# Kernel optimization log

Hardware: AMD Instinct MI355X
Metric: run time of the kernel (lower is better)

## Reference

```python
import jax, jax.numpy as jnp
import numpy as np

# dims
B_, L_, D_ = 2, 4096, 1024
E_ = 2
DIN = E_ * D_          # 2048 inner channels
P_ = 64                # d_head
H_ = DIN // P_         # 32 heads
N_ = 16                # d_state
K_ = 4                 # d_conv
DPROJ = 2 * DIN + 2 * N_ + H_   # z, u, B, C, dt
CONVD = DIN + 2 * N_            # conv over (u, B, C)


def rms(x, w, eps=1e-6):
    return x * jax.lax.rsqrt(jnp.mean(x * x, -1, keepdims=True) + eps) * w


def mixer(x, in_proj_w, conv_w, conv_b, A_param, dt_bias, D_skip, out_proj_w, out_proj_b):
    b, l, _ = x.shape
    proj = x @ in_proj_w.T                                   # (b,l,DPROJ)
    zgate, u, Bc, Cc, dt = jnp.split(proj, [DIN, 2 * DIN, 2 * DIN + N_, 2 * DIN + 2 * N_], axis=-1)
    # causal depthwise conv over (u,B,C), then SiLU
    xBC = jnp.concatenate([u, Bc, Cc], -1)                   # (b,l,CONVD)
    xt = jnp.pad(xBC.transpose(0, 2, 1), ((0, 0), (0, 0), (K_ - 1, 0)))
    conv = jax.lax.conv_general_dilated(xt, conv_w, (1,), 'VALID',
                                        feature_group_count=CONVD,
                                        dimension_numbers=('NCH', 'OIH', 'NCH'))
    xBC = jax.nn.silu(conv.transpose(0, 2, 1) + conv_b)
    u, Bc, Cc = jnp.split(xBC, [DIN, DIN + N_], axis=-1)
    # normalize_bc=True: L2-normalize B and C over the state dim
    Bc = Bc * jax.lax.rsqrt(jnp.sum(Bc * Bc, -1, keepdims=True) + 1e-6)
    Cc = Cc * jax.lax.rsqrt(jnp.sum(Cc * Cc, -1, keepdims=True) + 1e-6)
    dt = jax.nn.softplus(dt + dt_bias)                       # (b,l,H) selective step size
    A = jax.nn.relu(A_param)[None, :, None, :]               # (1,H,1,N) oscillator stiffness >= 0
    uh = u.reshape(b, l, H_, P_)

    def step(carry, inp):
        z, y = carry                                         # (b,H,P,N) each
        dt_t, B_t, C_t, u_t = inp
        d = dt_t[:, :, None, None]                           # (b,H,1,1)
        Bu = u_t[..., None] * B_t[:, None, None, :]          # (b,H,P,N)
        # LinOSS-IM implicit update (unconditionally stable)
        z = (z + d * (Bu - A * y)) / (1.0 + d * d * A)
        y = y + d * z
        out = jnp.einsum('bhpn,bn->bhp', y, C_t)
        return (z, y), out

    z0 = jnp.zeros((b, H_, P_, N_), x.dtype)
    seq = (dt.transpose(1, 0, 2), Bc.transpose(1, 0, 2), Cc.transpose(1, 0, 2), uh.transpose(1, 0, 2, 3))
    _, ys = jax.lax.scan(step, (z0, jnp.zeros_like(z0)), seq)  # (l,b,H,P)
    yout = ys.transpose(1, 0, 2, 3) + D_skip[None, None, :, None] * uh
    yout = yout.reshape(b, l, DIN) * jax.nn.silu(zgate)
    return yout @ out_proj_w.T + out_proj_b


def block_forward(x, norm1_w, in_proj_w, conv_w, conv_b, A_param, dt_bias, D_skip,
                  out_proj_w, out_proj_b, norm2_w, fc1_w, fc1_b, fc2_w, fc2_b):
    x = x + mixer(rms(x, norm1_w), in_proj_w, conv_w, conv_b, A_param, dt_bias,
                  D_skip, out_proj_w, out_proj_b)
    h = rms(x, norm2_w)
    h = jax.nn.gelu(h @ fc1_w.T + fc1_b, approximate=True)
    return x + h @ fc2_w.T + fc2_b


def setup_inputs() -> dict:
    key = jax.random.key(0)
    ks = jax.random.split(key, 16)
    s = lambda i, shape, sc=1.0: jax.random.normal(ks[i], shape, jnp.float32) * sc
    return dict(
        x=s(0, (B_, L_, D_)),
        norm1_w=jnp.ones((D_,), jnp.float32),
        in_proj_w=s(1, (DPROJ, D_), D_ ** -0.5),
        conv_w=s(2, (CONVD, 1, K_), 0.3),
        conv_b=jnp.zeros((CONVD,), jnp.float32),
        A_param=jax.random.uniform(ks[3], (H_, N_), jnp.float32),
        dt_bias=s(4, (H_,), 0.2) - 3.0,
        D_skip=s(5, (H_,), 0.1) + 1.0,
        out_proj_w=s(6, (D_, DIN), DIN ** -0.5),
        out_proj_b=jnp.zeros((D_,), jnp.float32),
        norm2_w=jnp.ones((D_,), jnp.float32),
        fc1_w=s(7, (4 * D_, D_), D_ ** -0.5),
        fc1_b=jnp.zeros((4 * D_,), jnp.float32),
        fc2_w=s(8, (D_, 4 * D_), (4 * D_) ** -0.5),
        fc2_b=jnp.zeros((D_,), jnp.float32),
    )


def reference(x, norm1_w, in_proj_w, conv_w, conv_b, A_param, dt_bias, D_skip,
              out_proj_w, out_proj_b, norm2_w, fc1_w, fc1_b, fc2_w, fc2_b):
    return block_forward(x, norm1_w, in_proj_w, conv_w, conv_b, A_param, dt_bias,
                         D_skip, out_proj_w, out_proj_b, norm2_w, fc1_w, fc1_b, fc2_w, fc2_b)
```

## Files before the change

### kernel.cpp

```cpp
#include <hip/hip_runtime.h>
#include <hip/hip_bf16.h>
#include <math.h>

#define B_ 2
#define L_ 4096
#define D_ 1024
#define DIN 2048
#define DPROJ 4160
#define CONVD 2080
#define H_ 32
#define P_ 64
#define N_ 16
#define K_ 4
#define M_ROWS (B_*L_)

#define NC 64
#define CH 64

typedef __bf16 bf16_8 __attribute__((ext_vector_type(8)));
typedef float f32x4 __attribute__((ext_vector_type(4)));

__device__ __forceinline__ void gload_lds16(const void* g, void* l) {
    __builtin_amdgcn_global_load_lds(
        (const __attribute__((address_space(1))) unsigned int*)g,
        (__attribute__((address_space(3))) unsigned int*)l, 16, 0, 0);
}

__global__ __launch_bounds__(256) void cvt_kernel(const float* __restrict__ src,
        __bf16* __restrict__ dst, int n) {
    int i = (blockIdx.x*256 + threadIdx.x)*8;
    if (i < n) {
        float4 f0 = *(const float4*)(src + i);
        float4 f1 = *(const float4*)(src + i + 4);
        bf16_8 o;
        o[0]=(__bf16)f0.x; o[1]=(__bf16)f0.y; o[2]=(__bf16)f0.z; o[3]=(__bf16)f0.w;
        o[4]=(__bf16)f1.x; o[5]=(__bf16)f1.y; o[6]=(__bf16)f1.z; o[7]=(__bf16)f1.w;
        *(bf16_8*)(dst + i) = o;
    }
}

template<typename TI>
__global__ __launch_bounds__(256) void rms_kernel(const TI* __restrict__ x,
        const float* __restrict__ w, __bf16* __restrict__ out) {
    int row = blockIdx.x;
    int tid = threadIdx.x;
    const TI* xr = x + (size_t)row * D_;
    float v[4];
    float ss = 0.f;
#pragma unroll
    for (int i = 0; i < 4; i++) {
        v[i] = (float)xr[tid*4 + i];
        ss += v[i]*v[i];
    }
#pragma unroll
    for (int off = 32; off >= 1; off >>= 1) ss += __shfl_xor(ss, off, 64);
    __shared__ float sred[4];
    int wave = tid >> 6;
    if ((tid & 63) == 0) sred[wave] = ss;
    __syncthreads();
    ss = sred[0] + sred[1] + sred[2] + sred[3];
    float scale = rsqrtf(ss * (1.f/(float)D_) + 1e-6f);
#pragma unroll
    for (int i = 0; i < 4; i++)
        out[(size_t)row*D_ + tid*4 + i] = (__bf16)(v[i] * scale * w[tid*4 + i]);
}

#define BM 128
#define BN 128
#define BK 64

template<int EPI>
__global__ __launch_bounds__(256) void gemm_kernel(
    const __bf16* __restrict__ A, const __bf16* __restrict__ W,
    void* __restrict__ Cout, const float* __restrict__ bias,
    const float* __restrict__ resid, int M, int N, int K)
{
    __shared__ __attribute__((aligned(16))) __bf16 As[2][BM][32];
    __shared__ __attribute__((aligned(16))) __bf16 Bs[2][BN][32];
    int tid = threadIdx.x;
    int lane = tid & 63, wave = tid >> 6;
    int wm = wave >> 1, wn = wave & 1;
    int quad = lane >> 4, l16 = lane & 15;

    int num_n = gridDim.x, num_m = gridDim.y;
    int pid = blockIdx.y * num_n + blockIdx.x;
    const int G = 8;
    int gsz = G * num_n;
    int grp = pid / gsz;
    int rem = pid - grp * gsz;
    int first_m = grp * G;
    int gm = (num_m - first_m < G) ? (num_m - first_m) : G;
    int m_idx = first_m + rem % gm;
    int n_idx = rem / gm;
    int bm0 = m_idx * BM, bn0 = n_idx * BN;

    int srow = lane >> 2;
    int sseg = lane & 3;

    f32x4 acc[4][4] = {};

    for (int kk = 0; kk < K; kk += BK) {
#pragma unroll
        for (int kh = 0; kh < 2; kh++) {
#pragma unroll
            for (int k = 0; k < 2; k++) {
                int c = wave*2 + k;
                int arow = bm0 + c*16 + srow;
                gload_lds16(A + (size_t)arow*K + kk + kh*32 + sseg*8,
                            (char*)&As[kh][0][0] + c*1024);
                int nr = bn0 + c*16 + srow;
                if (nr < N)
                    gload_lds16(W + (size_t)nr*K + kk + kh*32 + sseg*8,
                                (char*)&Bs[kh][0][0] + c*1024);
            }
        }
        __syncthreads();
#pragma unroll
        for (int kh = 0; kh < 2; kh++) {
            bf16_8 af[4], bfr[4];
#pragma unroll
            for (int i = 0; i < 4; i++) {
                af[i]  = *(const bf16_8*)&As[kh][wm*64 + i*16 + l16][quad*8];
                bfr[i] = *(const bf16_8*)&Bs[kh][wn*64 + i*16 + l16][quad*8];
            }
#pragma unroll
            for (int mi = 0; mi < 4; mi++)
#pragma unroll
                for (int ni = 0; ni < 4; ni++)
                    acc[mi][ni] = __builtin_amdgcn_mfma_f32_16x16x32_bf16(af[mi], bfr[ni], acc[mi][ni], 0, 0, 0);
        }
        __syncthreads();
    }

#pragma unroll
    for (int mi = 0; mi < 4; mi++) {
        int mbase = bm0 + wm*64 + mi*16 + quad*4;
#pragma unroll
        for (int ni = 0; ni < 4; ni++) {
            int n = bn0 + wn*64 + ni*16 + l16;
            if (n < N) {
#pragma unroll
                for (int r = 0; r < 4; r++) {
                    size_t idx = (size_t)(mbase + r)*N + n;
                    float v = acc[mi][ni][r];
                    if constexpr (EPI == 0) {
                        ((__bf16*)Cout)[idx] = (__bf16)v;
                    } else if constexpr (EPI == 2) {
                        v += bias[n] + resid[idx];
                        ((float*)Cout)[idx] = v;
                    } else if constexpr (EPI == 3) {
                        v += bias[n];
                        float u = 1.5957691216057308f*(v + 0.044715f*v*v*v);
                        float g = v * __builtin_amdgcn_rcpf(1.f + __expf(-u));
                        ((__bf16*)Cout)[idx] = (__bf16)g;
                    } else if constexpr (EPI == 4) {
                        v += bias[n] + resid[idx];
                        ((float*)Cout)[idx] = v;
                    }
                }
            }
        }
    }
}

__global__ __launch_bounds__(256) void conv_kernel(
    const __bf16* __restrict__ proj, const float* __restrict__ cw,
    const float* __restrict__ cb, __bf16* __restrict__ u_out,
    float* __restrict__ bc_out)
{
    const int NG = CONVD/8;
    int idx = blockIdx.x*256 + threadIdx.x;
    if (idx >= B_*(L_/4)*NG) return;
    int g  = idx % NG;
    int tg = idx / NG;
    int b  = tg / (L_/4);
    int t0 = (tg % (L_/4)) * 4;
    int c0 = g*8;
    size_t row0 = (size_t)b*L_ + t0;

    float4 w4[8];
#pragma unroll
    for (int q = 0; q < 8; q++)
        w4[q] = *(const float4*)&cw[c0*K_ + q*4];
    float4 cb0 = *(const float4*)&cb[c0];
    float4 cb1 = *(const float4*)&cb[c0 + 4];
    float cbv[8] = {cb0.x, cb0.y, cb0.z, cb0.w, cb1.x, cb1.y, cb1.z, cb1.w};

    float pv[7][8];
#pragma unroll
    for (int i = 0; i < 7; i++) {
        int r = t0 + i - 3;
        if (r >= 0) {
            bf16_8 v = *(const bf16_8*)&proj[((size_t)b*L_ + r)*DPROJ + DIN + c0];
#pragma unroll
            for (int j = 0; j < 8; j++) pv[i][j] = (float)v[j];
        } else {
#pragma unroll
            for (int j = 0; j < 8; j++) pv[i][j] = 0.f;
        }
    }

#pragma unroll
    for (int i = 0; i < 4; i++) {
        float s[8];
#pragma unroll
        for (int j = 0; j < 8; j++) {
            float acc = cbv[j];
#pragma unroll
            for (int k = 0; k < K_; k++)
                acc += pv[i + k][j] * w4[j][k];
            s[j] = acc / (1.f + __expf(-acc));
        }
        size_t row = row0 + i;
        if (c0 < DIN) {
            bf16_8 o;
#pragma unroll
            for (int j = 0; j < 8; j++) o[j] = (__bf16)s[j];
            *(bf16_8*)&u_out[row*DIN + c0] = o;
        } else {
            int cc = c0 - DIN;
            float4 f0 = {s[0], s[1], s[2], s[3]};
            float4 f1 = {s[4], s[5], s[6], s[7]};
            *(float4*)&bc_out[row*32 + cc]     = f0;
            *(float4*)&bc_out[row*32 + cc + 4] = f1;
        }
    }
}

__global__ __launch_bounds__(64) void prep_kernel(
    const float* __restrict__ bc, const __bf16* __restrict__ proj,
    const float* __restrict__ dt_bias,
    float* __restrict__ Bn, float* __restrict__ Cn, float* __restrict__ dtv)
{
    int row = blockIdx.x;
    int tid = threadIdx.x;
    if (tid < 32) {
        float v = bc[(size_t)row*32 + tid];
        float ss = v*v;
        ss += __shfl_xor(ss, 1, 16);
        ss += __shfl_xor(ss, 2, 16);
        ss += __shfl_xor(ss, 4, 16);
        ss += __shfl_xor(ss, 8, 16);
        float nv = v * rsqrtf(ss + 1e-6f);
        if (tid < 16) Bn[(size_t)row*16 + tid] = nv;
        else Cn[(size_t)row*16 + (tid-16)] = nv;
    } else {
        int h = tid - 32;
        float xv = (float)proj[(size_t)row*DPROJ + 2*DIN + 2*N_ + h] + dt_bias[h];
        float sp = (xv > 20.f) ? xv : log1pf(__expf(xv));
        dtv[(size_t)row*32 + h] = sp;
    }
}

__global__ __launch_bounds__(64) void scan_phase0(
    const float* __restrict__ dtv, const float* __restrict__ A_param,
    float* __restrict__ Mprod)
{
    int blk = blockIdx.x;
    int cg = blk & 15;
    int h  = (blk >> 4) & 31;
    int b  = blk >> 9;
    int lane = threadIdx.x;
    int n  = lane & 15;
    int c  = cg*4 + (lane >> 4);
    int bh = b*32 + h;

    float Av = fmaxf(A_param[h*16 + n], 0.f);
    float P00 = 1.f, P01 = 0.f, P10 = 0.f, P11 = 1.f;
    size_t r0 = (size_t)b*L_ + (size_t)c*CH;

#pragma unroll 4
    for (int tt = 0; tt < CH; tt++) {
        float d  = dtv[(r0 + tt)*32 + h];
        float rc = __builtin_amdgcn_rcpf(fmaf(d*d, Av, 1.f));
        float da = d*Av;
        float n00 = rc*fmaf(-da, P10, P00);
        float n01 = rc*fmaf(-da, P11, P01);
        float n10 = rc*fmaf(d, P00, P10);
        float n11 = rc*fmaf(d, P01, P11);
        P00=n00; P01=n01; P10=n10; P11=n11;
    }

    size_t mi = (((size_t)bh*NC + c)*16 + n)*4;
    Mprod[mi+0]=P00; Mprod[mi+1]=P01; Mprod[mi+2]=P10; Mprod[mi+3]=P11;
}

__global__ __launch_bounds__(64) void scan_phase1(
    const float* __restrict__ dtv, const float* __restrict__ Bn,
    const __bf16* __restrict__ u, const float* __restrict__ A_param,
    float* __restrict__ vbuf)
{
    __shared__ float rcT[CH][16];
    __shared__ float dT[CH];
    int blk = blockIdx.x;
    int c  = blk & (NC-1);
    int pg = (blk >> 6) & 3;
    int h  = (blk >> 8) & 31;
    int b  = blk >> 13;
    int lane = threadIdx.x;
    int pl = lane >> 2, nq = lane & 3;
    int p = pg*16 + pl;
    int ch = h*64 + p;
    int bh = b*32 + h;

    size_t r0 = (size_t)b*L_ + (size_t)c*CH;

    {
        float d = dtv[(r0 + lane)*32 + h];
        dT[lane] = d;
        float dd = d*d;
#pragma unroll
        for (int n = 0; n < 16; n++) {
            float Avn = fmaxf(A_param[h*16 + n], 0.f);
            rcT[lane][n] = __builtin_amdgcn_rcpf(fmaf(dd, Avn, 1.f));
        }
    }
    __syncthreads();

    float Av[4];
#pragma unroll
    for (int j = 0; j < 4; j++) Av[j] = fmaxf(A_param[h*16 + nq*4 + j], 0.f);

    float z[4] = {}, y[4] = {};

#pragma unroll 8
    for (int tt = 0; tt < CH; tt++) {
        size_t rn = r0 + tt;
        float d  = dT[tt];
        float4 rc4 = *(const float4*)&rcT[tt][nq*4];
        float4 Bv = *(const float4*)&Bn[rn*16 + nq*4];
        float up = (float)u[rn*DIN + ch];
        float rcj[4] = {rc4.x, rc4.y, rc4.z, rc4.w};
        float Bvj[4] = {Bv.x, Bv.y, Bv.z, Bv.w};
#pragma unroll
        for (int j = 0; j < 4; j++) {
            float q = fmaf(-Av[j], y[j], up*Bvj[j]);
            float zn = fmaf(d, q, z[j]) * rcj[j];
            z[j] = zn;
            y[j] = fmaf(d, zn, y[j]);
        }
    }

    size_t vb = ((size_t)bh*NC + c)*16;
#pragma unroll
    for (int j = 0; j < 4; j++) {
        int n = nq*4 + j;
        size_t vi = ((vb + n)*64 + p)*2;
        vbuf[vi]   = z[j];
        vbuf[vi+1] = y[j];
    }
}

__global__ __launch_bounds__(64) void scan_phase2(
    float* __restrict__ vbuf, const float* __restrict__ Mprod)
{
    int blk = blockIdx.x;
    int bh = blk >> 4;
    int n  = blk & 15;
    int p = threadIdx.x;
    float z = 0.f, y = 0.f;
#pragma unroll 4
    for (int c = 0; c < NC; c++) {
        size_t base = ((size_t)bh*NC + c)*16 + n;
        float4 mm = *(const float4*)&Mprod[base*4];
        size_t vi = (base*64 + p)*2;
        float vz = vbuf[vi], vy = vbuf[vi+1];
        vbuf[vi]   = z;
        vbuf[vi+1] = y;
        float zn = mm.x*z + mm.y*y + vz;
        float yn = mm.z*z + mm.w*y + vy;
        z = zn; y = yn;
    }
}

__global__ __launch_bounds__(64) void scan_phase3(
    const float* __restrict__ dtv, const float* __restrict__ Bn,
    const float* __restrict__ Cn, const __bf16* __restrict__ u,
    const __bf16* __restrict__ proj, const float* __restrict__ A_param,
    const float* __restrict__ D_skip, const float* __restrict__ vbuf,
    __bf16* __restrict__ y2)
{
    __shared__ float rcT[CH][16];
    __shared__ float dT[CH];
    int blk = blockIdx.x;
    int c  = blk & (NC-1);
    int pg = (blk >> 6) & 3;
    int h  = (blk >> 8) & 31;
    int b  = blk >> 13;
    int lane = threadIdx.x;
    int pl = lane >> 2, nq = lane & 3;
    int p = pg*16 + pl;
    int ch = h*64 + p;
    int bh = b*32 + h;

    size_t r0 = (size_t)b*L_ + (size_t)c*CH;

    {
        float d = dtv[(r0 + lane)*32 + h];
        dT[lane] = d;
        float dd = d*d;
#pragma unroll
        for (int n = 0; n < 16; n++) {
            float Avn = fmaxf(A_param[h*16 + n], 0.f);
            rcT[lane][n] = __builtin_amdgcn_rcpf(fmaf(dd, Avn, 1.f));
        }
    }
    __syncthreads();

    float Av[4];
#pragma unroll
    for (int j = 0; j < 4; j++) Av[j] = fmaxf(A_param[h*16 + nq*4 + j], 0.f);
    float Dsk = D_skip[h];

    float z[4], y[4];
    size_t vb = ((size_t)bh*NC + c)*16;
#pragma unroll
    for (int j = 0; j < 4; j++) {
        int n = nq*4 + j;
        size_t vi = ((vb + n)*64 + p)*2;
        z[j] = vbuf[vi];
        y[j] = vbuf[vi+1];
    }

#pragma unroll 8
    for (int tt = 0; tt < CH; tt++) {
        size_t rn = r0 + tt;
        float d  = dT[tt];
        float4 rc4 = *(const float4*)&rcT[tt][nq*4];
        float4 Bv = *(const float4*)&Bn[rn*16 + nq*4];
        float4 Cv = *(const float4*)&Cn[rn*16 + nq*4];
        float up = (float)u[rn*DIN + ch];
        float zg = (float)proj[rn*DPROJ + ch];
        float rcj[4] = {rc4.x, rc4.y, rc4.z, rc4.w};
        float Bvj[4] = {Bv.x, Bv.y, Bv.z, Bv.w};
        float Cvj[4] = {Cv.x, Cv.y, Cv.z, Cv.w};
        float s = 0.f;
#pragma unroll
        for (int j = 0; j < 4; j++) {
            float q = fmaf(-Av[j], y[j], up*Bvj[j]);
            float zn = fmaf(d, q, z[j]) * rcj[j];
            z[j] = zn;
            y[j] = fmaf(d, zn, y[j]);
            s = fmaf(y[j], Cvj[j], s);
        }
        s += __shfl_xor(s, 1, 64);
        s += __shfl_xor(s, 2, 64);
        if (nq == 0) {
            float sig = __builtin_amdgcn_rcpf(1.f + __expf(-zg));
            y2[rn*DIN + ch] = (__bf16)((s + Dsk*up) * (zg * sig));
        }
    }
}

extern "C" void kernel_launch(void* const* d_in, const int* in_sizes, int n_in,
                              void* d_out, int out_size, void* d_ws, size_t ws_size,
                              hipStream_t stream) {
    const float* x         = (const float*)d_in[0];
    const float* norm1_w   = (const float*)d_in[1];
    const float* in_proj_w = (const float*)d_in[2];
    const float* conv_w    = (const float*)d_in[3];
    const float* conv_b    = (const float*)d_in[4];
    const float* A_param   = (const float*)d_in[5];
    const float* dt_bias   = (const float*)d_in[6];
    const float* D_skip    = (const float*)d_in[7];
    const float* out_proj_w= (const float*)d_in[8];
    const float* out_proj_b= (const float*)d_in[9];
    const float* norm2_w   = (const float*)d_in[10];
    const float* fc1_w     = (const float*)d_in[11];
    const float* fc1_b     = (const float*)d_in[12];
    const float* fc2_w     = (const float*)d_in[13];
    const float* fc2_b     = (const float*)d_in[14];
    float* out = (float*)d_out;

    char* ws = (char*)d_ws;
    const size_t R0 = 0;
    const size_t R0_SZ = (size_t)M_ROWS*DPROJ*2;
    const size_t R1 = R0_SZ;
    const size_t R1_SZ = (size_t)M_ROWS*4*D_*2;
    const size_t R2 = R1 + R1_SZ;

    __bf16* proj   = (__bf16*)(ws + R0);
    float*  x2     = (float*) (ws + R0);
    __bf16* x2n    = (__bf16*)(ws + R0 + (size_t)M_ROWS*D_*4);
    __bf16* xn     = (__bf16*)(ws + R1);
    __bf16* y2     = (__bf16*)(ws + R1);
    __bf16* u_conv = (__bf16*)(ws + R1 + (size_t)M_ROWS*DIN*2);
    __bf16* h1     = (__bf16*)(ws + R1);
    float*  bcraw  = (float*)(ws + R2);
    float*  Bn     = (float*)(ws + R2 + (size_t)M_ROWS*32*4);
    float*  Cn     = (float*)(ws + R2 + (size_t)M_ROWS*32*4 + (size_t)M_ROWS*16*4);
    float*  dtv    = (float*)(ws + R2 + (size_t)M_ROWS*32*4 + (size_t)M_ROWS*16*4*2);
    float*  Mprod  = (float*)(ws + R2 + (size_t)M_ROWS*32*4*2 + (size_t)M_ROWS*16*4*2);
    __bf16* Wb     = (__bf16*)(ws + R2 + (size_t)M_ROWS*32*4*2 + (size_t)M_ROWS*16*4*2
                                 + (size_t)64*64*16*4*4);

    float* vbuf = (float*)d_out;

    rms_kernel<float><<<M_ROWS, 256, 0, stream>>>(x, norm1_w, xn);

    {
        int n = DPROJ*D_;
        cvt_kernel<<<(n/8 + 255)/256, 256, 0, stream>>>(in_proj_w, Wb, n);
        dim3 grid((DPROJ + BN - 1)/BN, M_ROWS/BM);
        gemm_kernel<0><<<grid, 256, 0, stream>>>(xn, Wb, proj, nullptr, nullptr,
                                                 M_ROWS, DPROJ, D_);
    }

    {
        int total = B_*(L_/4)*(CONVD/8);
        conv_kernel<<<(total + 255)/256, 256, 0, stream>>>(proj, conv_w, conv_b, u_conv, bcraw);
    }

    prep_kernel<<<M_ROWS, 64, 0, stream>>>(bcraw, proj, dt_bias, Bn, Cn, dtv);

    {
        int full = B_*H_*4*NC;
        scan_phase0<<<B_*H_*16, 64, 0, stream>>>(dtv, A_param, Mprod);
        scan_phase1<<<full, 64, 0, stream>>>(dtv, Bn, u_conv, A_param, vbuf);
        scan_phase2<<<B_*H_*16, 64, 0, stream>>>(vbuf, Mprod);
        scan_phase3<<<full, 64, 0, stream>>>(dtv, Bn, Cn, u_conv, proj, A_param, D_skip,
                                             vbuf, y2);
    }

    {
        int n = D_*DIN;
        cvt_kernel<<<(n/8 + 255)/256, 256, 0, stream>>>(out_proj_w, Wb, n);
        dim3 grid((D_ + BN - 1)/BN, M_ROWS/BM);
        gemm_kernel<2><<<grid, 256, 0, stream>>>(y2, Wb, x2, out_proj_b, x, M_ROWS, D_, DIN);
    }

    rms_kernel<float><<<M_ROWS, 256, 0, stream>>>(x2, norm2_w, x2n);

    {
        int n = 4*D_*D_;
        cvt_kernel<<<(n/8 + 255)/256, 256, 0, stream>>>(fc1_w, Wb, n);
        dim3 grid((4*D_ + BN - 1)/BN, M_ROWS/BM);
        gemm_kernel<3><<<grid, 256, 0, stream>>>(x2n, Wb, h1, fc1_b, nullptr, M_ROWS, 4*D_, D_);
    }

    {
        int n = D_*4*D_;
        cvt_kernel<<<(n/8 + 255)/256, 256, 0, stream>>>(fc2_w, Wb, n);
        dim3 grid((D_ + BN - 1)/BN, M_ROWS/BM);
        gemm_kernel<4><<<grid, 256, 0, stream>>>(h1, Wb, out, fc2_b, x2, M_ROWS, D_, 4*D_);
    }
}
```

Baseline: 697.1 us.

## Give each scan thread all 16 states of one channel, staging B/C in LDS

Scan phases 1 and 3 now assign one thread per head channel holding all 16 state elements in registers, instead of four threads each holding four states. This removes the cross-lane shuffle reduction and makes every lane do the output store. B and C are staged into padded shared-memory tiles once per chunk rather than read from global memory on every timestep. The grid shrinks fourfold to 4096 blocks of 64 threads, which lowers parallelism and raises register pressure per thread in exchange for less redundant u/z loads and less shuffle work.

```diff
diff --git a/kernel.cpp b/kernel.cpp
--- a/kernel.cpp
+++ b/kernel.cpp
@@ -16,6 +16,7 @@
 
 #define NC 64
 #define CH 64
+#define TP 20
 
 typedef __bf16 bf16_8 __attribute__((ext_vector_type(8)));
 typedef float f32x4 __attribute__((ext_vector_type(4)));
@@ -290,64 +291,77 @@
     const __bf16* __restrict__ u, const float* __restrict__ A_param,
     float* __restrict__ vbuf)
 {
-    __shared__ float rcT[CH][16];
+    __shared__ float rcT[CH][TP];
+    __shared__ float BT[CH][TP];
     __shared__ float dT[CH];
     int blk = blockIdx.x;
     int c  = blk & (NC-1);
-    int pg = (blk >> 6) & 3;
-    int h  = (blk >> 8) & 31;
-    int b  = blk >> 13;
+    int h  = (blk >> 6) & 31;
+    int b  = blk >> 11;
     int lane = threadIdx.x;
-    int pl = lane >> 2, nq = lane & 3;
-    int p = pg*16 + pl;
-    int ch = h*64 + p;
+    int ch = h*64 + lane;
     int bh = b*32 + h;
 
     size_t r0 = (size_t)b*L_ + (size_t)c*CH;
 
-    {
-        float d = dtv[(r0 + lane)*32 + h];
-        dT[lane] = d;
+    float Av[16];
+#pragma unroll
+    for (int g = 0; g < 4; g++) {
+        float4 a4 = *(const float4*)&A_param[h*16 + g*4];
+        Av[g*4+0] = fmaxf(a4.x, 0.f); Av[g*4+1] = fmaxf(a4.y, 0.f);
+        Av[g*4+2] = fmaxf(a4.z, 0.f); Av[g*4+3] = fmaxf(a4.w, 0.f);
+    }
+
+    {
+        int tt = lane;
+        size_t rn = r0 + tt;
+        float d = dtv[rn*32 + h];
+        dT[tt] = d;
         float dd = d*d;
 #pragma unroll
-        for (int n = 0; n < 16; n++) {
-            float Avn = fmaxf(A_param[h*16 + n], 0.f);
-            rcT[lane][n] = __builtin_amdgcn_rcpf(fmaf(dd, Avn, 1.f));
+        for (int g = 0; g < 4; g++) {
+            float4 b4 = *(const float4*)&Bn[rn*16 + g*4];
+            *(float4*)&BT[tt][g*4] = b4;
+            float4 r4;
+            r4.x = __builtin_amdgcn_rcpf(fmaf(dd, Av[g*4+0], 1.f));
+            r4.y = __builtin_amdgcn_rcpf(fmaf(dd, Av[g*4+1], 1.f));
+            r4.z = __builtin_amdgcn_rcpf(fmaf(dd, Av[g*4+2], 1.f));
+            r4.w = __builtin_amdgcn_rcpf(fmaf(dd, Av[g*4+3], 1.f));
+            *(float4*)&rcT[tt][g*4] = r4;
         }
     }
     __syncthreads();
 
-    float Av[4];
-#pragma unroll
-    for (int j = 0; j < 4; j++) Av[j] = fmaxf(A_param[h*16 + nq*4 + j], 0.f);
-
-    float z[4] = {}, y[4] = {};
-
-#pragma unroll 8
+    float z[16] = {}, y[16] = {};
+
+#pragma unroll 4
     for (int tt = 0; tt < CH; tt++) {
         size_t rn = r0 + tt;
         float d  = dT[tt];
-        float4 rc4 = *(const float4*)&rcT[tt][nq*4];
-        float4 Bv = *(const float4*)&Bn[rn*16 + nq*4];
         float up = (float)u[rn*DIN + ch];
-        float rcj[4] = {rc4.x, rc4.y, rc4.z, rc4.w};
-        float Bvj[4] = {Bv.x, Bv.y, Bv.z, Bv.w};
-#pragma unroll
-        for (int j = 0; j < 4; j++) {
-            float q = fmaf(-Av[j], y[j], up*Bvj[j]);
-            float zn = fmaf(d, q, z[j]) * rcj[j];
-            z[j] = zn;
-            y[j] = fmaf(d, zn, y[j]);
+#pragma unroll
+        for (int g = 0; g < 4; g++) {
+            float4 B4  = *(const float4*)&BT[tt][g*4];
+            float4 rc4 = *(const float4*)&rcT[tt][g*4];
+            float Bj[4]  = {B4.x, B4.y, B4.z, B4.w};
+            float rcj[4] = {rc4.x, rc4.y, rc4.z, rc4.w};
+#pragma unroll
+            for (int j = 0; j < 4; j++) {
+                int n = g*4 + j;
+                float q = fmaf(-Av[n], y[n], up*Bj[j]);
+                float zn = fmaf(d, q, z[n]) * rcj[j];
+                z[n] = zn;
+                y[n] = fmaf(d, zn, y[n]);
+            }
         }
     }
 
     size_t vb = ((size_t)bh*NC + c)*16;
 #pragma unroll
-    for (int j = 0; j < 4; j++) {
-        int n = nq*4 + j;
-        size_t vi = ((vb + n)*64 + p)*2;
-        vbuf[vi]   = z[j];
-        vbuf[vi+1] = y[j];
+    for (int n = 0; n < 16; n++) {
+        size_t vi = ((vb + n)*64 + lane)*2;
+        vbuf[vi]   = z[n];
+        vbuf[vi+1] = y[n];
     }
 }
 
@@ -380,75 +394,87 @@
     const float* __restrict__ D_skip, const float* __restrict__ vbuf,
     __bf16* __restrict__ y2)
 {
-    __shared__ float rcT[CH][16];
+    __shared__ float rcT[CH][TP];
+    __shared__ float BT[CH][TP];
+    __shared__ float CT[CH][TP];
     __shared__ float dT[CH];
     int blk = blockIdx.x;
     int c  = blk & (NC-1);
-    int pg = (blk >> 6) & 3;
-    int h  = (blk >> 8) & 31;
-    int b  = blk >> 13;
+    int h  = (blk >> 6) & 31;
+    int b  = blk >> 11;
     int lane = threadIdx.x;
-    int pl = lane >> 2, nq = lane & 3;
-    int p = pg*16 + pl;
-    int ch = h*64 + p;
+    int ch = h*64 + lane;
     int bh = b*32 + h;
 
     size_t r0 = (size_t)b*L_ + (size_t)c*CH;
 
-    {
-        float d = dtv[(r0 + lane)*32 + h];
-        dT[lane] = d;
+    float Av[16];
+#pragma unroll
+    for (int g = 0; g < 4; g++) {
+        float4 a4 = *(const float4*)&A_param[h*16 + g*4];
+        Av[g*4+0] = fmaxf(a4.x, 0.f); Av[g*4+1] = fmaxf(a4.y, 0.f);
+        Av[g*4+2] = fmaxf(a4.z, 0.f); Av[g*4+3] = fmaxf(a4.w, 0.f);
+    }
+    float Dsk = D_skip[h];
+
+    {
+        int tt = lane;
+        size_t rn = r0 + tt;
+        float d = dtv[rn*32 + h];
+        dT[tt] = d;
         float dd = d*d;
 #pragma unroll
-        for (int n = 0; n < 16; n++) {
-            float Avn = fmaxf(A_param[h*16 + n], 0.f);
-            rcT[lane][n] = __builtin_amdgcn_rcpf(fmaf(dd, Avn, 1.f));
+        for (int g = 0; g < 4; g++) {
+            float4 b4 = *(const float4*)&Bn[rn*16 + g*4];
+            float4 c4 = *(const float4*)&Cn[rn*16 + g*4];
+            *(float4*)&BT[tt][g*4] = b4;
+            *(float4*)&CT[tt][g*4] = c4;
+            float4 r4;
+            r4.x = __builtin_amdgcn_rcpf(fmaf(dd, Av[g*4+0], 1.f));
+            r4.y = __builtin_amdgcn_rcpf(fmaf(dd, Av[g*4+1], 1.f));
+            r4.z = __builtin_amdgcn_rcpf(fmaf(dd, Av[g*4+2], 1.f));
+            r4.w = __builtin_amdgcn_rcpf(fmaf(dd, Av[g*4+3], 1.f));
+            *(float4*)&rcT[tt][g*4] = r4;
         }
     }
     __syncthreads();
 
-    float Av[4];
-#pragma unroll
-    for (int j = 0; j < 4; j++) Av[j] = fmaxf(A_param[h*16 + nq*4 + j], 0.f);
-    float Dsk = D_skip[h];
-
-    float z[4], y[4];
+    float z[16], y[16];
     size_t vb = ((size_t)bh*NC + c)*16;
 #pragma unroll
-    for (int j = 0; j < 4; j++) {
-        int n = nq*4 + j;
-        size_t vi = ((vb + n)*64 + p)*2;
-        z[j] = vbuf[vi];
-        y[j] = vbuf[vi+1];
-    }
-
-#pragma unroll 8
+    for (int n = 0; n < 16; n++) {
+        size_t vi = ((vb + n)*64 + lane)*2;
+        z[n] = vbuf[vi];
+        y[n] = vbuf[vi+1];
+    }
+
+#pragma unroll 4
     for (int tt = 0; tt < CH; tt++) {
         size_t rn = r0 + tt;
         float d  = dT[tt];
-        float4 rc4 = *(const float4*)&rcT[tt][nq*4];
-        float4 Bv = *(const float4*)&Bn[rn*16 + nq*4];
-        float4 Cv = *(const float4*)&Cn[rn*16 + nq*4];
         float up = (float)u[rn*DIN + ch];
         float zg = (float)proj[rn*DPROJ + ch];
-        float rcj[4] = {rc4.x, rc4.y, rc4.z, rc4.w};
-        float Bvj[4] = {Bv.x, Bv.y, Bv.z, Bv.w};
-        float Cvj[4] = {Cv.x, Cv.y, Cv.z, Cv.w};
         float s = 0.f;
 #pragma unroll
-        for (int j = 0; j < 4; j++) {
-            float q = fmaf(-Av[j], y[j], up*Bvj[j]);
-            float zn = fmaf(d, q, z[j]) * rcj[j];
-            z[j] = zn;
-            y[j] = fmaf(d, zn, y[j]);
-            s = fmaf(y[j], Cvj[j], s);
-        }
-        s += __shfl_xor(s, 1, 64);
-        s += __shfl_xor(s, 2, 64);
-        if (nq == 0) {
-            float sig = __builtin_amdgcn_rcpf(1.f + __expf(-zg));
-            y2[rn*DIN + ch] = (__bf16)((s + Dsk*up) * (zg * sig));
-        }
+        for (int g = 0; g < 4; g++) {
+            float4 B4  = *(const float4*)&BT[tt][g*4];
+            float4 C4  = *(const float4*)&CT[tt][g*4];
+            float4 rc4 = *(const float4*)&rcT[tt][g*4];
+            float Bj[4]  = {B4.x, B4.y, B4.z, B4.w};
+            float Cj[4]  = {C4.x, C4.y, C4.z, C4.w};
+            float rcj[4] = {rc4.x, rc4.y, rc4.z, rc4.w};
+#pragma unroll
+            for (int j = 0; j < 4; j++) {
+                int n = g*4 + j;
+                float q = fmaf(-Av[n], y[n], up*Bj[j]);
+                float zn = fmaf(d, q, z[n]) * rcj[j];
+                z[n] = zn;
+                y[n] = fmaf(d, zn, y[n]);
+                s = fmaf(y[n], Cj[j], s);
+            }
+        }
+        float sig = __builtin_amdgcn_rcpf(1.f + __expf(-zg));
+        y2[rn*DIN + ch] = (__bf16)((s + Dsk*up) * (zg * sig));
     }
 }
 
@@ -514,7 +540,7 @@
     prep_kernel<<<M_ROWS, 64, 0, stream>>>(bcraw, proj, dt_bias, Bn, Cn, dtv);
 
     {
-        int full = B_*H_*4*NC;
+        int full = B_*H_*NC;
         scan_phase0<<<B_*H_*16, 64, 0, stream>>>(dtv, A_param, Mprod);
         scan_phase1<<<full, 64, 0, stream>>>(dtv, Bn, u_conv, A_param, vbuf);
         scan_phase2<<<B_*H_*16, 64, 0, stream>>>(vbuf, Mprod);
```

Result: faster. 626.1 us (-10.2%).
